# Kernel tuning notes

Hardware: AMD Instinct MI355X
Metric: run time of the kernel (lower is better)

The kernel has to match this reference:

```python
import jax, jax.numpy as jnp
import numpy as np
import math

HIDDEN = 1024
INTER = 4096
HEADS = 16
HEAD_DIM = 64
INNER = HEADS * HEAD_DIM
SEQ = 4096


def setup_inputs() -> dict:
    key = jax.random.key(0)
    ks = jax.random.split(key, 16)
    s = 0.02
    d = dict(
        x=jax.random.normal(ks[0], (SEQ, HIDDEN), dtype=jnp.float32),
        # attention norm
        an_w=jnp.ones((HIDDEN,), jnp.float32),
        an_b=jnp.zeros((HIDDEN,), jnp.float32),
        # attention projections (weight stored as [out, in] like torch)
        q_w=jax.random.normal(ks[1], (INNER, HIDDEN)) * s,
        q_b=jnp.zeros((INNER,), jnp.float32),
        k_w=jax.random.normal(ks[2], (INNER, HIDDEN)) * s,
        k_b=jnp.zeros((INNER,), jnp.float32),
        v_w=jax.random.normal(ks[3], (INNER, HIDDEN)) * s,
        v_b=jnp.zeros((INNER,), jnp.float32),
        o_w=jax.random.normal(ks[4], (HIDDEN, INNER)) * s,
        o_b=jnp.zeros((HIDDEN,), jnp.float32),
        # ff norm
        fn_w=jnp.ones((HIDDEN,), jnp.float32),
        fn_b=jnp.zeros((HIDDEN,), jnp.float32),
        ff1_w=jax.random.normal(ks[5], (INTER, HIDDEN)) * s,
        ff1_b=jnp.zeros((INTER,), jnp.float32),
        ff2_w=jax.random.normal(ks[6], (HIDDEN, INTER)) * s,
        ff2_b=jnp.zeros((HIDDEN,), jnp.float32),
    )
    return d


def _norm_novar(x, w, b):
    # mean-only layer norm (no variance normalization)
    return w * (x - jnp.mean(x, axis=-1, keepdims=True)) + b


def _block(x, an_w, an_b, q_w, q_b, k_w, k_b, v_w, v_b, o_w, o_b,
           fn_w, fn_b, ff1_w, ff1_b, ff2_w, ff2_b):
    S = x.shape[0]
    scale = math.sqrt(HEAD_DIM)
    xn = _norm_novar(x, an_w, an_b)
    # [S, inner] -> [h, S, d]
    Q = (xn @ q_w.T + q_b).reshape(S, HEADS, HEAD_DIM).transpose(1, 0, 2)
    K = (xn @ k_w.T + k_b).reshape(S, HEADS, HEAD_DIM).transpose(1, 0, 2)
    V = (xn @ v_w.T + v_b).reshape(S, HEADS, HEAD_DIM).transpose(1, 0, 2)
    scores = jnp.einsum('hsd,htd->hst', Q, K) / scale  # [h, S, S]
    attn = jax.nn.softmax(scores, axis=-1)
    ctx = jnp.einsum('hst,htd->hsd', attn, V)  # [h, S, d]
    ctx = ctx.transpose(1, 0, 2).reshape(S, INNER)
    x = ctx @ o_w.T + o_b + x
    xn = _norm_novar(x, fn_w, fn_b)
    h = jax.nn.relu(xn @ ff1_w.T + ff1_b)
    return h @ ff2_w.T + ff2_b + x


def reference(x, an_w, an_b, q_w, q_b, k_w, k_b, v_w, v_b, o_w, o_b,
              fn_w, fn_b, ff1_w, ff1_b, ff2_w, ff2_b):
    return _block(x, an_w, an_b, q_w, q_b, k_w, k_b, v_w, v_b, o_w, o_b,
                  fn_w, fn_b, ff1_w, ff1_b, ff2_w, ff2_b)
```

## Files before the change

kernel.cpp:

```cpp
#include <hip/hip_runtime.h>
#include <hip/hip_bf16.h>

#define SQ 4096
#define HID 1024
#define INTER_DIM 4096
#define NH 16
#define DH 64
#define SCALE_Q 0.18033688f

typedef __attribute__((ext_vector_type(4))) float f32x4;
typedef __attribute__((ext_vector_type(16))) float f32x16;
typedef __attribute__((ext_vector_type(8))) short bf16x8;

__device__ __forceinline__ unsigned short f2bf(float f) {
  union { float f; unsigned int i; } v; v.f = f;
  unsigned int i = v.i;
  return (unsigned short)((i + 0x7FFFu + ((i >> 16) & 1u)) >> 16);
}

__device__ __forceinline__ void load_lds16(const void* g, void* l) {
  __builtin_amdgcn_global_load_lds(
      (const __attribute__((address_space(1))) void*)g,
      (__attribute__((address_space(3))) void*)l, 16, 0, 0);
}

__device__ __forceinline__ int cvtpk_bf16(float a, float b) {
  int r;
  asm("v_cvt_pk_bf16_f32 %0, %1, %2" : "=v"(r) : "v"(a), "v"(b));
  return r;
}

__global__ __launch_bounds__(256) void cvt6_kernel(
    const float* __restrict__ s0, const float* __restrict__ s1,
    const float* __restrict__ s2, const float* __restrict__ s3,
    const float* __restrict__ s4, const float* __restrict__ s5,
    unsigned short* __restrict__ dst) {
  const int b = blockIdx.x;
  const float* src;
  int lb;
  size_t base4;
  if (b < 4096) {
    const int r = b >> 10;
    lb = b & 1023;
    src = (r == 0) ? s0 : (r == 1) ? s1 : (r == 2) ? s2 : s3;
    base4 = (size_t)r << 18;
  } else if (b < 8192) {
    lb = b - 4096; src = s4; base4 = 1u << 20;
  } else {
    lb = b - 8192; src = s5; base4 = 2u << 20;
  }
  const float sc = (b < 1024) ? SCALE_Q : 1.0f;
  const int i = lb * 256 + threadIdx.x;
  const float4 v4 = ((const float4*)src)[i];
  ushort4 o4;
  o4.x = f2bf(v4.x * sc); o4.y = f2bf(v4.y * sc);
  o4.z = f2bf(v4.z * sc); o4.w = f2bf(v4.w * sc);
  ((ushort4*)dst)[base4 + i] = o4;
}

__global__ __launch_bounds__(256) void bias3_kernel(
    const float* __restrict__ qb, const float* __restrict__ kb,
    const float* __restrict__ vb, float* __restrict__ dst) {
  const int b = blockIdx.x, t = threadIdx.x;
  const float* s = (b == 0) ? qb : (b == 1) ? kb : vb;
  float4 v = ((const float4*)s)[t];
  if (b == 0) { v.x *= SCALE_Q; v.y *= SCALE_Q; v.z *= SCALE_Q; v.w *= SCALE_Q; }
  ((float4*)dst)[b * 256 + t] = v;
}

__global__ __launch_bounds__(256) void ln_kernel(
    const float* __restrict__ x, const float* __restrict__ w,
    const float* __restrict__ b, unsigned short* __restrict__ out) {
  const int row = blockIdx.x;
  const int t = threadIdx.x;
  const float4 v = ((const float4*)(x + (size_t)row * HID))[t];
  float s = v.x + v.y + v.z + v.w;
  #pragma unroll
  for (int off = 32; off > 0; off >>= 1) s += __shfl_xor(s, off);
  __shared__ float red[4];
  if ((t & 63) == 0) red[t >> 6] = s;
  __syncthreads();
  const float mean = (red[0] + red[1] + red[2] + red[3]) * (1.0f / HID);
  const float4 wv = ((const float4*)w)[t];
  const float4 bv = ((const float4*)b)[t];
  ushort4 o;
  o.x = f2bf(wv.x * (v.x - mean) + bv.x);
  o.y = f2bf(wv.y * (v.y - mean) + bv.y);
  o.z = f2bf(wv.z * (v.z - mean) + bv.z);
  o.w = f2bf(wv.w * (v.w - mean) + bv.w);
  ((ushort4*)(out + (size_t)row * HID))[t] = o;
}

template <int MODE>
__global__ __launch_bounds__(256) void gemm_bt(
    const unsigned short* __restrict__ A, const unsigned short* __restrict__ B,
    const float* __restrict__ bias, const float* __restrict__ res,
    void* __restrict__ Cout, void* __restrict__ Cout2, int M, int N, int K) {
  __shared__ __align__(16) unsigned short As[2][128 * 32];
  __shared__ __align__(16) unsigned short Bs[2][128 * 32];
  const int t = threadIdx.x;
  const int lane = t & 63;
  const int wave = t >> 6;
  const int g = lane >> 4;
  const int lr = lane & 15;
  const int waveM = wave >> 1, waveN = wave & 1;
  const int rowBase = blockIdx.x * 128;
  const int colBase = blockIdx.y * 128;

  f32x4 acc[4][4];
  #pragma unroll
  for (int m = 0; m < 4; ++m)
    #pragma unroll
    for (int n = 0; n < 4; ++n) acc[m][n] = (f32x4){0.f, 0.f, 0.f, 0.f};

  const int c0 = t, c1 = t + 256;
  const int r0s = c0 >> 2, s0 = (c0 & 3) ^ (r0s & 3);
  const int r1s = c1 >> 2, s1 = (c1 & 3) ^ (r1s & 3);
  const unsigned short* gA0 = A + (size_t)(rowBase + r0s) * K + s0 * 8;
  const unsigned short* gA1 = A + (size_t)(rowBase + r1s) * K + s1 * 8;
  const unsigned short* gB0 = B + (size_t)(colBase + r0s) * K + s0 * 8;
  const unsigned short* gB1 = B + (size_t)(colBase + r1s) * K + s1 * 8;

  load_lds16(gA0, &As[0][wave * 512]);
  load_lds16(gA1, &As[0][2048 + wave * 512]);
  load_lds16(gB0, &Bs[0][wave * 512]);
  load_lds16(gB1, &Bs[0][2048 + wave * 512]);
  __syncthreads();

  const int nk = K >> 5;
  for (int kt = 0; kt < nk; ++kt) {
    const int buf = kt & 1;
    if (kt + 1 < nk) {
      const int k0 = (kt + 1) << 5;
      load_lds16(gA0 + k0, &As[buf ^ 1][wave * 512]);
      load_lds16(gA1 + k0, &As[buf ^ 1][2048 + wave * 512]);
      load_lds16(gB0 + k0, &Bs[buf ^ 1][wave * 512]);
      load_lds16(gB1 + k0, &Bs[buf ^ 1][2048 + wave * 512]);
    }
    bf16x8 af[4], bfr[4];
    #pragma unroll
    for (int m = 0; m < 4; ++m) {
      const int r = waveM * 64 + m * 16 + lr;
      af[m] = *(const bf16x8*)&As[buf][r * 32 + ((g ^ (r & 3)) << 3)];
    }
    #pragma unroll
    for (int n = 0; n < 4; ++n) {
      const int c = waveN * 64 + n * 16 + lr;
      bfr[n] = *(const bf16x8*)&Bs[buf][c * 32 + ((g ^ (c & 3)) << 3)];
    }
    #pragma unroll
    for (int m = 0; m < 4; ++m)
      #pragma unroll
      for (int n = 0; n < 4; ++n)
        acc[m][n] = __builtin_amdgcn_mfma_f32_16x16x32_bf16(af[m], bfr[n],
                                                            acc[m][n], 0, 0, 0);
    __syncthreads();
  }

  const int crow0 = rowBase + waveM * 64;
  const int ccol0 = colBase + waveN * 64;
  #pragma unroll
  for (int n = 0; n < 4; ++n) {
    const int col = ccol0 + n * 16 + lr;
    const float bv = bias[col];
    #pragma unroll
    for (int m = 0; m < 4; ++m) {
      const int row0 = crow0 + m * 16 + g * 4;
      if (MODE == 4) {
        if (col < 2048) {
          #pragma unroll
          for (int j = 0; j < 4; ++j)
            ((unsigned short*)Cout)[(size_t)(row0 + j) * 2048 + col] =
                f2bf(acc[m][n][j] + bv);
        } else {
          ushort4 o4;
          o4.x = f2bf(acc[m][n][0] + bv);
          o4.y = f2bf(acc[m][n][1] + bv);
          o4.z = f2bf(acc[m][n][2] + bv);
          o4.w = f2bf(acc[m][n][3] + bv);
          *(ushort4*)&((unsigned short*)Cout2)[(size_t)(col - 2048) * M + row0] = o4;
        }
      } else if (MODE == 1) {
        #pragma unroll
        for (int j = 0; j < 4; ++j)
          ((unsigned short*)Cout)[(size_t)(row0 + j) * N + col] =
              f2bf(fmaxf(acc[m][n][j] + bv, 0.f));
      } else {
        #pragma unroll
        for (int j = 0; j < 4; ++j)
          ((float*)Cout)[(size_t)(row0 + j) * N + col] =
              acc[m][n][j] + bv + res[(size_t)(row0 + j) * N + col];
      }
    }
  }
}

__global__ __launch_bounds__(256, 2) void attn_kernel(
    const unsigned short* __restrict__ QK,
    const unsigned short* __restrict__ Vt,
    unsigned short* __restrict__ ctx) {
  const int s = blockIdx.y * gridDim.x + blockIdx.x;
  const int q6 = s >> 3;
  const int h = (s & 7) * 2 + (q6 >> 5);
  const int qt = q6 & 31;

  const int t = threadIdx.x;
  const int lane = t & 63;
  const int wave = t >> 6;
  const int ql = lane & 31;
  const int hi = lane >> 5;

  __shared__ __align__(16) unsigned short Ks[2][64 * 64];
  __shared__ __align__(16) unsigned short Vs[2][64 * 64];

  const int qbase = qt * 128 + wave * 32;
  const unsigned short* qptr =
      QK + (size_t)(qbase + ql) * 2048 + h * DH + hi * 8;
  bf16x8 qf[4];
  #pragma unroll
  for (int ks = 0; ks < 4; ++ks) qf[ks] = *(const bf16x8*)(qptr + ks * 16);

  const int cr = t >> 3, cs = t & 7;
  const int cr2 = cr + 32;
  const unsigned short* gK0 =
      QK + (size_t)cr * 2048 + 1024 + h * DH + ((cs ^ (cr & 7)) << 3);
  const unsigned short* gK1 =
      QK + (size_t)cr2 * 2048 + 1024 + h * DH + ((cs ^ (cr2 & 7)) << 3);
  const unsigned short* gV0 = Vt + (size_t)(h * DH + cr) * SQ + ((cs ^ (cr & 7)) << 3);
  const unsigned short* gV1 = Vt + (size_t)(h * DH + cr2) * SQ + ((cs ^ (cr2 & 7)) << 3);

  float mreg = 0.f, lreg = 0.f;
  f32x16 oacc0 = 0.f, oacc1 = 0.f;

  load_lds16(gK0, &Ks[0][wave * 512]);
  load_lds16(gK1, &Ks[0][2048 + wave * 512]);
  load_lds16(gV0, &Vs[0][wave * 512]);
  load_lds16(gV1, &Vs[0][2048 + wave * 512]);

  for (int kt = 0; kt < SQ / 64; ++kt) {
    const int buf = kt & 1;
    __syncthreads();
    if (kt + 1 < SQ / 64) {
      const size_t ko = (size_t)(kt + 1) * 64 * 2048;
      const int vo = (kt + 1) * 64;
      load_lds16(gK0 + ko, &Ks[buf ^ 1][wave * 512]);
      load_lds16(gK1 + ko, &Ks[buf ^ 1][2048 + wave * 512]);
      load_lds16(gV0 + vo, &Vs[buf ^ 1][wave * 512]);
      load_lds16(gV1 + vo, &Vs[buf ^ 1][2048 + wave * 512]);
    }
    const unsigned short* KsB = &Ks[buf][0];
    const unsigned short* VsB = &Vs[buf][0];

    f32x16 st0, st1;
    #pragma unroll
    for (int r = 0; r < 16; ++r) { st0[r] = -mreg; st1[r] = -mreg; }
    __builtin_amdgcn_s_setprio(1);
    #pragma unroll
    for (int ks = 0; ks < 4; ++ks) {
      const int sl = ((((ks << 1) | hi) ^ (ql & 7)) << 3);
      const bf16x8 k0 = *(const bf16x8*)&KsB[ql * 64 + sl];
      const bf16x8 k1 = *(const bf16x8*)&KsB[(32 + ql) * 64 + sl];
      st0 = __builtin_amdgcn_mfma_f32_32x32x16_bf16(k0, qf[ks], st0, 0, 0, 0);
      st1 = __builtin_amdgcn_mfma_f32_32x32x16_bf16(k1, qf[ks], st1, 0, 0, 0);
    }
    __builtin_amdgcn_s_setprio(0);

    bf16x8 vf0[4], vf1[4];
    #pragma unroll
    for (int ks = 0; ks < 4; ++ks) {
      const int sl = ((((ks << 1) | hi) ^ (ql & 7)) << 3);
      vf0[ks] = *(const bf16x8*)&VsB[ql * 64 + sl];
      vf1[ks] = *(const bf16x8*)&VsB[(32 + ql) * 64 + sl];
    }

    float tr[16];
    #pragma unroll
    for (int r = 0; r < 16; ++r) tr[r] = fmaxf(st0[r], st1[r]);
    #pragma unroll
    for (int s2 = 8; s2 > 0; s2 >>= 1)
      #pragma unroll
      for (int r = 0; r < s2; ++r) tr[r] = fmaxf(tr[r], tr[r + s2]);
    const float mx = fmaxf(tr[0], __shfl_xor(tr[0], 32));

    if (!__all(mx <= 8.0f)) {
      const float mpos = fmaxf(mx, 0.f);
      const float corr = exp2f(-mpos);
      mreg += mpos;
      lreg *= corr;
      #pragma unroll
      for (int r = 0; r < 16; ++r) { st0[r] -= mpos; st1[r] -= mpos; }
      #pragma unroll
      for (int r = 0; r < 16; ++r) {
        const float c = __shfl(corr, (r & 3) + 8 * (r >> 2) + 4 * hi);
        oacc0[r] *= c;
        oacc1[r] *= c;
      }
    }

    #pragma unroll
    for (int r = 0; r < 16; ++r) st0[r] = exp2f(st0[r]);
    #pragma unroll
    for (int r = 0; r < 16; ++r) st1[r] = exp2f(st1[r]);
    float ts[16];
    #pragma unroll
    for (int r = 0; r < 16; ++r) ts[r] = st0[r] + st1[r];
    #pragma unroll
    for (int s2 = 8; s2 > 0; s2 >>= 1)
      #pragma unroll
      for (int r = 0; r < s2; ++r) ts[r] += ts[r + s2];
    lreg += ts[0] + __shfl_xor(ts[0], 32);

    union { int w[4]; bf16x8 v; } pa[4];
    #pragma unroll
    for (int half = 0; half < 2; ++half) {
      #pragma unroll
      for (int kk = 0; kk < 2; ++kk) {
        const int base = kk * 8;
        float p0, p1, p2, p3, p4, p5, p6, p7;
        if (half == 0) {
          p0 = st0[base + 0]; p1 = st0[base + 1]; p2 = st0[base + 2]; p3 = st0[base + 3];
          p4 = st0[base + 4]; p5 = st0[base + 5]; p6 = st0[base + 6]; p7 = st0[base + 7];
        } else {
          p0 = st1[base + 0]; p1 = st1[base + 1]; p2 = st1[base + 2]; p3 = st1[base + 3];
          p4 = st1[base + 4]; p5 = st1[base + 5]; p6 = st1[base + 6]; p7 = st1[base + 7];
        }
        const int d0 = cvtpk_bf16(p0, p1), sw0 = cvtpk_bf16(p4, p5);
        const int d1 = cvtpk_bf16(p2, p3), sw1 = cvtpk_bf16(p6, p7);
        auto a = __builtin_amdgcn_permlane32_swap(d0, sw0, false, false);
        auto b = __builtin_amdgcn_permlane32_swap(d1, sw1, false, false);
        const int ks = half * 2 + kk;
        pa[ks].w[0] = a[0]; pa[ks].w[1] = b[0];
        pa[ks].w[2] = a[1]; pa[ks].w[3] = b[1];
      }
    }

    __builtin_amdgcn_s_setprio(1);
    #pragma unroll
    for (int ks = 0; ks < 4; ++ks) {
      oacc0 = __builtin_amdgcn_mfma_f32_32x32x16_bf16(pa[ks].v, vf0[ks], oacc0, 0, 0, 0);
      oacc1 = __builtin_amdgcn_mfma_f32_32x32x16_bf16(pa[ks].v, vf1[ks], oacc1, 0, 0, 0);
    }
    __builtin_amdgcn_s_setprio(0);
  }

  const float linv = 1.0f / lreg;
  #pragma unroll
  for (int r = 0; r < 16; ++r) {
    const int qq = (r & 3) + 8 * (r >> 2) + 4 * hi;
    const float li = __shfl(linv, qq);
    unsigned short* cp = ctx + (size_t)(qbase + qq) * HID + h * DH + ql;
    cp[0] = f2bf(oacc0[r] * li);
    cp[32] = f2bf(oacc1[r] * li);
  }
}

extern "C" void kernel_launch(void* const* d_in, const int* in_sizes, int n_in,
                              void* d_out, int out_size, void* d_ws,
                              size_t ws_size, hipStream_t stream) {
  const float* x     = (const float*)d_in[0];
  const float* an_w  = (const float*)d_in[1];
  const float* an_b  = (const float*)d_in[2];
  const float* q_w   = (const float*)d_in[3];
  const float* q_b   = (const float*)d_in[4];
  const float* k_w   = (const float*)d_in[5];
  const float* k_b   = (const float*)d_in[6];
  const float* v_w   = (const float*)d_in[7];
  const float* v_b   = (const float*)d_in[8];
  const float* o_w   = (const float*)d_in[9];
  const float* o_b   = (const float*)d_in[10];
  const float* fn_w  = (const float*)d_in[11];
  const float* fn_b  = (const float*)d_in[12];
  const float* ff1_w = (const float*)d_in[13];
  const float* ff1_b = (const float*)d_in[14];
  const float* ff2_w = (const float*)d_in[15];
  const float* ff2_b = (const float*)d_in[16];

  char* ws = (char*)d_ws;
  const size_t MB = 1ull << 20;
  unsigned short* xn    = (unsigned short*)(ws + 0);
  unsigned short* qkvwb = (unsigned short*)(ws + 8 * MB);
  unsigned short* owb   = (unsigned short*)(ws + 14 * MB);
  unsigned short* f1wb  = (unsigned short*)(ws + 16 * MB);
  unsigned short* f2wb  = (unsigned short*)(ws + 24 * MB);
  unsigned short* QKm   = (unsigned short*)(ws + 32 * MB);
  unsigned short* Vtm   = (unsigned short*)(ws + 48 * MB);
  unsigned short* ctx   = (unsigned short*)(ws + 56 * MB);
  float*          bAll  = (float*)(ws + 56 * MB);
  float*          x2    = (float*)(ws + 64 * MB);
  unsigned short* hbuf  = (unsigned short*)(ws + 32 * MB);
  unsigned short* x2n   = xn;

  cvt6_kernel<<<12288, 256, 0, stream>>>(q_w, k_w, v_w, o_w, ff1_w, ff2_w, qkvwb);
  bias3_kernel<<<3, 256, 0, stream>>>(q_b, k_b, v_b, bAll);

  ln_kernel<<<SQ, 256, 0, stream>>>(x, an_w, an_b, xn);

  gemm_bt<4><<<dim3(SQ / 128, 3072 / 128), 256, 0, stream>>>(
      xn, qkvwb, bAll, nullptr, QKm, Vtm, SQ, 3072, HID);

  attn_kernel<<<dim3(32, 16), 256, 0, stream>>>(QKm, Vtm, ctx);

  gemm_bt<2><<<dim3(SQ / 128, HID / 128), 256, 0, stream>>>(
      ctx, owb, o_b, x, x2, nullptr, SQ, HID, HID);

  ln_kernel<<<SQ, 256, 0, stream>>>(x2, fn_w, fn_b, x2n);

  gemm_bt<1><<<dim3(SQ / 128, INTER_DIM / 128), 256, 0, stream>>>(
      x2n, f1wb, ff1_b, nullptr, hbuf, nullptr, SQ, INTER_DIM, HID);

  gemm_bt<2><<<dim3(SQ / 128, HID / 128), 256, 0, stream>>>(
      hbuf, f2wb, ff2_b, x2, (float*)d_out, nullptr, SQ, HID, INTER_DIM);
}
```

Before: 446.7 us.

## Use 256x256 GEMM tiles, split-KV attention and split-K FF2 with combine kernels

Replaces the 128x128 GEMMs for QKV and FF1 with 512-thread 256x256 tiles built on 32x32x16 MFMA. Attention is split into two KV halves, each writing unnormalized bf16 partials plus max/sum, and a combine kernel merges them. FF2 uses split-K=4 with bf16 partials, combined together with the residual. Raw v_exp_f32 replaces exp2f. This adds extra kernels and memory traffic, and bf16-rounded partials cost some accuracy in exchange for more parallelism and data reuse.

```diff
diff --git a/kernel.cpp b/kernel.cpp
--- a/kernel.cpp
+++ b/kernel.cpp
@@ -12,6 +12,9 @@
 typedef __attribute__((ext_vector_type(16))) float f32x16;
 typedef __attribute__((ext_vector_type(8))) short bf16x8;
 
+__device__ __forceinline__ float bf2f(unsigned short u) {
+  union { float f; unsigned int i; } v; v.i = ((unsigned int)u) << 16; return v.f;
+}
 __device__ __forceinline__ unsigned short f2bf(float f) {
   union { float f; unsigned int i; } v; v.f = f;
   unsigned int i = v.i;
@@ -27,6 +30,12 @@
 __device__ __forceinline__ int cvtpk_bf16(float a, float b) {
   int r;
   asm("v_cvt_pk_bf16_f32 %0, %1, %2" : "=v"(r) : "v"(a), "v"(b));
+  return r;
+}
+
+__device__ __forceinline__ float fexp2(float x) {
+  float r;
+  asm("v_exp_f32 %0, %1\n\ts_nop 1" : "=v"(r) : "v"(x));
   return r;
 }
 
@@ -92,10 +101,139 @@
 }
 
 template <int MODE>
-__global__ __launch_bounds__(256) void gemm_bt(
+__global__ __launch_bounds__(512, 1) void gemm256(
+    const unsigned short* __restrict__ A, const unsigned short* __restrict__ B,
+    const float* __restrict__ bias, void* __restrict__ C0,
+    void* __restrict__ C1, int M, int N, int K) {
+  __shared__ __align__(16) unsigned short As[2][8192];
+  __shared__ __align__(16) unsigned short Bs[2][8192];
+  const int t = threadIdx.x;
+  const int lane = t & 63;
+  const int w = t >> 6;
+  const int ql = lane & 31, hi = lane >> 5;
+  const int wm = w >> 2, wn = w & 3;
+  const int bR = blockIdx.x * 256;
+  const int bC = blockIdx.y * 256;
+  const int Keff = (MODE == 6) ? (K >> 2) : K;
+  const int kBase = (MODE == 6) ? blockIdx.z * Keff : 0;
+
+  f32x16 acc[4][2];
+  #pragma unroll
+  for (int mf = 0; mf < 4; ++mf)
+    #pragma unroll
+    for (int nf = 0; nf < 2; ++nf) acc[mf][nf] = 0.f;
+
+  const int r0 = t >> 2, s0 = (t & 3) ^ (r0 & 3);
+  const int r1 = r0 + 128, s1 = (t & 3) ^ (r1 & 3);
+  const unsigned short* gA0 = A + (size_t)(bR + r0) * K + kBase + s0 * 8;
+  const unsigned short* gA1 = A + (size_t)(bR + r1) * K + kBase + s1 * 8;
+  const unsigned short* gB0 = B + (size_t)(bC + r0) * K + kBase + s0 * 8;
+  const unsigned short* gB1 = B + (size_t)(bC + r1) * K + kBase + s1 * 8;
+
+  load_lds16(gA0, &As[0][w * 512]);
+  load_lds16(gA1, &As[0][4096 + w * 512]);
+  load_lds16(gB0, &Bs[0][w * 512]);
+  load_lds16(gB1, &Bs[0][4096 + w * 512]);
+  __syncthreads();
+
+  const int nk = Keff >> 5;
+  for (int kt = 0; kt < nk; ++kt) {
+    const int buf = kt & 1;
+    if (kt + 1 < nk) {
+      const int k0 = (kt + 1) << 5;
+      load_lds16(gA0 + k0, &As[buf ^ 1][w * 512]);
+      load_lds16(gA1 + k0, &As[buf ^ 1][4096 + w * 512]);
+      load_lds16(gB0 + k0, &Bs[buf ^ 1][w * 512]);
+      load_lds16(gB1 + k0, &Bs[buf ^ 1][4096 + w * 512]);
+    }
+    bf16x8 af[2][4], bfr[2][2];
+    #pragma unroll
+    for (int ks = 0; ks < 2; ++ks) {
+      #pragma unroll
+      for (int mf = 0; mf < 4; ++mf) {
+        const int row = wm * 128 + mf * 32 + ql;
+        af[ks][mf] = *(const bf16x8*)
+            &As[buf][row * 32 + ((ks * 16 + hi * 8) ^ ((row & 3) << 3))];
+      }
+      #pragma unroll
+      for (int nf = 0; nf < 2; ++nf) {
+        const int col = wn * 64 + nf * 32 + ql;
+        bfr[ks][nf] = *(const bf16x8*)
+            &Bs[buf][col * 32 + ((ks * 16 + hi * 8) ^ ((col & 3) << 3))];
+      }
+    }
+    __builtin_amdgcn_s_setprio(1);
+    #pragma unroll
+    for (int ks = 0; ks < 2; ++ks)
+      #pragma unroll
+      for (int mf = 0; mf < 4; ++mf)
+        #pragma unroll
+        for (int nf = 0; nf < 2; ++nf)
+          acc[mf][nf] = __builtin_amdgcn_mfma_f32_32x32x16_bf16(
+              af[ks][mf], bfr[ks][nf], acc[mf][nf], 0, 0, 0);
+    __builtin_amdgcn_s_setprio(0);
+    __syncthreads();
+  }
+
+  #pragma unroll
+  for (int mf = 0; mf < 4; ++mf) {
+    #pragma unroll
+    for (int nf = 0; nf < 2; ++nf) {
+      const int col = bC + wn * 64 + nf * 32 + ql;
+      const float bv = bias[col];
+      const int rowb = bR + wm * 128 + mf * 32;
+      if (MODE == 4) {
+        if (col < 2048) {
+          #pragma unroll
+          for (int r = 0; r < 16; ++r) {
+            const int row = rowb + (r & 3) + 8 * (r >> 2) + 4 * hi;
+            ((unsigned short*)C0)[(size_t)row * 2048 + col] =
+                f2bf(acc[mf][nf][r] + bv);
+          }
+        } else {
+          #pragma unroll
+          for (int r2 = 0; r2 < 4; ++r2) {
+            const int row = rowb + 8 * r2 + 4 * hi;
+            ushort4 o4;
+            o4.x = f2bf(acc[mf][nf][4 * r2 + 0] + bv);
+            o4.y = f2bf(acc[mf][nf][4 * r2 + 1] + bv);
+            o4.z = f2bf(acc[mf][nf][4 * r2 + 2] + bv);
+            o4.w = f2bf(acc[mf][nf][4 * r2 + 3] + bv);
+            *(ushort4*)&((unsigned short*)C1)[(size_t)(col - 2048) * M + row] = o4;
+          }
+        }
+      } else if (MODE == 1) {
+        #pragma unroll
+        for (int r = 0; r < 16; ++r) {
+          const int row = rowb + (r & 3) + 8 * (r >> 2) + 4 * hi;
+          ((unsigned short*)C0)[(size_t)row * N + col] =
+              f2bf(fmaxf(acc[mf][nf][r] + bv, 0.f));
+        }
+      } else {
+        if (blockIdx.z == 3) {
+          #pragma unroll
+          for (int r = 0; r < 16; ++r) {
+            const int row = rowb + (r & 3) + 8 * (r >> 2) + 4 * hi;
+            ((float*)C0)[(size_t)row * N + col] = acc[mf][nf][r] + bv;
+          }
+        } else {
+          unsigned short* P =
+              (unsigned short*)C1 + (size_t)blockIdx.z * M * (size_t)N;
+          #pragma unroll
+          for (int r = 0; r < 16; ++r) {
+            const int row = rowb + (r & 3) + 8 * (r >> 2) + 4 * hi;
+            P[(size_t)row * N + col] = f2bf(acc[mf][nf][r]);
+          }
+        }
+      }
+    }
+  }
+}
+
+__global__ __launch_bounds__(256) void gemm128_res(
     const unsigned short* __restrict__ A, const unsigned short* __restrict__ B,
     const float* __restrict__ bias, const float* __restrict__ res,
-    void* __restrict__ Cout, void* __restrict__ Cout2, int M, int N, int K) {
+    float* __restrict__ Cout, int M, int N, int K) {
   __shared__ __align__(16) unsigned short As[2][128 * 32];
   __shared__ __align__(16) unsigned short Bs[2][128 * 32];
   const int t = threadIdx.x;
@@ -165,43 +303,26 @@
     const float bv = bias[col];
     #pragma unroll
     for (int m = 0; m < 4; ++m) {
-      const int row0 = crow0 + m * 16 + g * 4;
-      if (MODE == 4) {
-        if (col < 2048) {
-          #pragma unroll
-          for (int j = 0; j < 4; ++j)
-            ((unsigned short*)Cout)[(size_t)(row0 + j) * 2048 + col] =
-                f2bf(acc[m][n][j] + bv);
-        } else {
-          ushort4 o4;
-          o4.x = f2bf(acc[m][n][0] + bv);
-          o4.y = f2bf(acc[m][n][1] + bv);
-          o4.z = f2bf(acc[m][n][2] + bv);
-          o4.w = f2bf(acc[m][n][3] + bv);
-          *(ushort4*)&((unsigned short*)Cout2)[(size_t)(col - 2048) * M + row0] = o4;
-        }
-      } else if (MODE == 1) {
-        #pragma unroll
-        for (int j = 0; j < 4; ++j)
-          ((unsigned short*)Cout)[(size_t)(row0 + j) * N + col] =
-              f2bf(fmaxf(acc[m][n][j] + bv, 0.f));
-      } else {
-        #pragma unroll
-        for (int j = 0; j < 4; ++j)
-          ((float*)Cout)[(size_t)(row0 + j) * N + col] =
-              acc[m][n][j] + bv + res[(size_t)(row0 + j) * N + col];
+      #pragma unroll
+      for (int j = 0; j < 4; ++j) {
+        const int row = crow0 + m * 16 + g * 4 + j;
+        Cout[(size_t)row * N + col] =
+            acc[m][n][j] + bv + res[(size_t)row * N + col];
       }
     }
   }
 }
 
-__global__ __launch_bounds__(256, 2) void attn_kernel(
+__global__ __launch_bounds__(256, 4) void attn_kernel(
     const unsigned short* __restrict__ QK,
     const unsigned short* __restrict__ Vt,
-    unsigned short* __restrict__ ctx) {
+    unsigned short* __restrict__ ctxP,
+    float2* __restrict__ ml) {
   const int s = blockIdx.y * gridDim.x + blockIdx.x;
-  const int q6 = s >> 3;
-  const int h = (s & 7) * 2 + (q6 >> 5);
+  const int kvh = s & 1;
+  const int s2 = s >> 1;
+  const int q6 = s2 >> 3;
+  const int h = (s2 & 7) * 2 + (q6 >> 5);
   const int qt = q6 & 31;
 
   const int t = threadIdx.x;
@@ -222,12 +343,15 @@
 
   const int cr = t >> 3, cs = t & 7;
   const int cr2 = cr + 32;
+  const size_t kvoff = (size_t)kvh * 2048;
   const unsigned short* gK0 =
-      QK + (size_t)cr * 2048 + 1024 + h * DH + ((cs ^ (cr & 7)) << 3);
+      QK + (kvoff + cr) * 2048 + 1024 + h * DH + ((cs ^ (cr & 7)) << 3);
   const unsigned short* gK1 =
-      QK + (size_t)cr2 * 2048 + 1024 + h * DH + ((cs ^ (cr2 & 7)) << 3);
-  const unsigned short* gV0 = Vt + (size_t)(h * DH + cr) * SQ + ((cs ^ (cr & 7)) << 3);
-  const unsigned short* gV1 = Vt + (size_t)(h * DH + cr2) * SQ + ((cs ^ (cr2 & 7)) << 3);
+      QK + (kvoff + cr2) * 2048 + 1024 + h * DH + ((cs ^ (cr2 & 7)) << 3);
+  const unsigned short* gV0 =
+      Vt + (size_t)(h * DH + cr) * SQ + kvoff + ((cs ^ (cr & 7)) << 3);
+  const unsigned short* gV1 =
+      Vt + (size_t)(h * DH + cr2) * SQ + kvoff + ((cs ^ (cr2 & 7)) << 3);
 
   float mreg = 0.f, lreg = 0.f;
   f32x16 oacc0 = 0.f, oacc1 = 0.f;
@@ -237,10 +361,11 @@
   load_lds16(gV0, &Vs[0][wave * 512]);
   load_lds16(gV1, &Vs[0][2048 + wave * 512]);
 
-  for (int kt = 0; kt < SQ / 64; ++kt) {
+  const int NT = 32;
+  for (int kt = 0; kt < NT; ++kt) {
     const int buf = kt & 1;
     __syncthreads();
-    if (kt + 1 < SQ / 64) {
+    if (kt + 1 < NT) {
       const size_t ko = (size_t)(kt + 1) * 64 * 2048;
       const int vo = (kt + 1) * 64;
       load_lds16(gK0 + ko, &Ks[buf ^ 1][wave * 512]);
@@ -277,14 +402,14 @@
     #pragma unroll
     for (int r = 0; r < 16; ++r) tr[r] = fmaxf(st0[r], st1[r]);
     #pragma unroll
-    for (int s2 = 8; s2 > 0; s2 >>= 1)
-      #pragma unroll
-      for (int r = 0; r < s2; ++r) tr[r] = fmaxf(tr[r], tr[r + s2]);
+    for (int s2_ = 8; s2_ > 0; s2_ >>= 1)
+      #pragma unroll
+      for (int r = 0; r < s2_; ++r) tr[r] = fmaxf(tr[r], tr[r + s2_]);
     const float mx = fmaxf(tr[0], __shfl_xor(tr[0], 32));
 
     if (!__all(mx <= 8.0f)) {
       const float mpos = fmaxf(mx, 0.f);
-      const float corr = exp2f(-mpos);
+      const float corr = fexp2(-mpos);
       mreg += mpos;
       lreg *= corr;
       #pragma unroll
@@ -298,16 +423,16 @@
     }
 
     #pragma unroll
-    for (int r = 0; r < 16; ++r) st0[r] = exp2f(st0[r]);
-    #pragma unroll
-    for (int r = 0; r < 16; ++r) st1[r] = exp2f(st1[r]);
+    for (int r = 0; r < 16; ++r) st0[r] = fexp2(st0[r]);
+    #pragma unroll
+    for (int r = 0; r < 16; ++r) st1[r] = fexp2(st1[r]);
     float ts[16];
     #pragma unroll
     for (int r = 0; r < 16; ++r) ts[r] = st0[r] + st1[r];
     #pragma unroll
-    for (int s2 = 8; s2 > 0; s2 >>= 1)
-      #pragma unroll
-      for (int r = 0; r < s2; ++r) ts[r] += ts[r + s2];
+    for (int s2_ = 8; s2_ > 0; s2_ >>= 1)
+      #pragma unroll
+      for (int r = 0; r < s2_; ++r) ts[r] += ts[r + s2_];
     lreg += ts[0] + __shfl_xor(ts[0], 32);
 
     union { int w[4]; bf16x8 v; } pa[4];
@@ -343,15 +468,66 @@
     __builtin_amdgcn_s_setprio(0);
   }
 
-  const float linv = 1.0f / lreg;
+  unsigned short* cpb = ctxP + (size_t)kvh * (SQ * (size_t)HID);
   #pragma unroll
   for (int r = 0; r < 16; ++r) {
     const int qq = (r & 3) + 8 * (r >> 2) + 4 * hi;
-    const float li = __shfl(linv, qq);
-    unsigned short* cp = ctx + (size_t)(qbase + qq) * HID + h * DH + ql;
-    cp[0] = f2bf(oacc0[r] * li);
-    cp[32] = f2bf(oacc1[r] * li);
-  }
+    unsigned short* cp = cpb + (size_t)(qbase + qq) * HID + h * DH + ql;
+    cp[0] = f2bf(oacc0[r]);
+    cp[32] = f2bf(oacc1[r]);
+  }
+  if (hi == 0) {
+    float2 v; v.x = mreg; v.y = lreg;
+    ml[(size_t)kvh * (SQ * NH) + (size_t)(qbase + ql) * NH + h] = v;
+  }
+}
+
+__global__ __launch_bounds__(256) void combine2_kernel(
+    const unsigned short* __restrict__ ctxP, const float2* __restrict__ ml,
+    unsigned short* __restrict__ ctx) {
+  const int i = blockIdx.x * 256 + threadIdx.x;
+  const int row = i >> 7;
+  const int dc = (i & 127) * 8;
+  const int head = dc >> 6;
+  const float2 a = ml[(size_t)row * NH + head];
+  const float2 b = ml[(size_t)(SQ + row) * NH + head];
+  const float M = fmaxf(a.x, b.x);
+  const float w0 = fexp2(a.x - M), w1 = fexp2(b.x - M);
+  const float inv = 1.0f / (w0 * a.y + w1 * b.y);
+  const size_t off = (size_t)row * HID + dc;
+  const size_t P = (size_t)SQ * HID;
+  ushort4 p0a = *(const ushort4*)&ctxP[off];
+  ushort4 p0b = *(const ushort4*)&ctxP[off + 4];
+  ushort4 p1a = *(const ushort4*)&ctxP[P + off];
+  ushort4 p1b = *(const ushort4*)&ctxP[P + off + 4];
+  ushort4 oa, ob;
+  oa.x = f2bf((w0 * bf2f(p0a.x) + w1 * bf2f(p1a.x)) * inv);
+  oa.y = f2bf((w0 * bf2f(p0a.y) + w1 * bf2f(p1a.y)) * inv);
+  oa.z = f2bf((w0 * bf2f(p0a.z) + w1 * bf2f(p1a.z)) * inv);
+  oa.w = f2bf((w0 * bf2f(p0a.w) + w1 * bf2f(p1a.w)) * inv);
+  ob.x = f2bf((w0 * bf2f(p0b.x) + w1 * bf2f(p1b.x)) * inv);
+  ob.y = f2bf((w0 * bf2f(p0b.y) + w1 * bf2f(p1b.y)) * inv);
+  ob.z = f2bf((w0 * bf2f(p0b.z) + w1 * bf2f(p1b.z)) * inv);
+  ob.w = f2bf((w0 * bf2f(p0b.w) + w1 * bf2f(p1b.w)) * inv);
+  *(ushort4*)&ctx[off] = oa;
+  *(ushort4*)&ctx[off + 4] = ob;
+}
+
+__global__ __launch_bounds__(256) void combine4_kernel(
+    float* __restrict__ out, const unsigned short* __restrict__ parts,
+    const float* __restrict__ res) {
+  const int i = blockIdx.x * 256 + threadIdx.x;
+  const size_t P = (size_t)SQ * HID;
+  float4 o = ((const float4*)out)[i];
+  const float4 r = ((const float4*)res)[i];
+  const ushort4 a = ((const ushort4*)parts)[i];
+  const ushort4 b = ((const ushort4*)(parts + P))[i];
+  const ushort4 c = ((const ushort4*)(parts + 2 * P))[i];
+  o.x += r.x + bf2f(a.x) + bf2f(b.x) + bf2f(c.x);
+  o.y += r.y + bf2f(a.y) + bf2f(b.y) + bf2f(c.y);
+  o.z += r.z + bf2f(a.z) + bf2f(b.z) + bf2f(c.z);
+  o.w += r.w + bf2f(a.w) + bf2f(b.w) + bf2f(c.w);
+  ((float4*)out)[i] = o;
 }
 
 extern "C" void kernel_launch(void* const* d_in, const int* in_sizes, int n_in,
@@ -378,6 +554,7 @@
   char* ws = (char*)d_ws;
   const size_t MB = 1ull << 20;
   unsigned short* xn    = (unsigned short*)(ws + 0);
+  float2*         mlb   = (float2*)(ws + 0);
   unsigned short* qkvwb = (unsigned short*)(ws + 8 * MB);
   unsigned short* owb   = (unsigned short*)(ws + 14 * MB);
   unsigned short* f1wb  = (unsigned short*)(ws + 16 * MB);
@@ -387,27 +564,33 @@
   unsigned short* ctx   = (unsigned short*)(ws + 56 * MB);
   float*          bAll  = (float*)(ws + 56 * MB);
   float*          x2    = (float*)(ws + 64 * MB);
+  unsigned short* ctxP  = (unsigned short*)(ws + 64 * MB);
   unsigned short* hbuf  = (unsigned short*)(ws + 32 * MB);
   unsigned short* x2n   = xn;
+  unsigned short* parts = (unsigned short*)(ws + 0);
 
   cvt6_kernel<<<12288, 256, 0, stream>>>(q_w, k_w, v_w, o_w, ff1_w, ff2_w, qkvwb);
   bias3_kernel<<<3, 256, 0, stream>>>(q_b, k_b, v_b, bAll);
 
   ln_kernel<<<SQ, 256, 0, stream>>>(x, an_w, an_b, xn);
 
-  gemm_bt<4><<<dim3(SQ / 128, 3072 / 128), 256, 0, stream>>>(
-      xn, qkvwb, bAll, nullptr, QKm, Vtm, SQ, 3072, HID);
-
-  attn_kernel<<<dim3(32, 16), 256, 0, stream>>>(QKm, Vtm, ctx);
-
-  gemm_bt<2><<<dim3(SQ / 128, HID / 128), 256, 0, stream>>>(
-      ctx, owb, o_b, x, x2, nullptr, SQ, HID, HID);
+  gemm256<4><<<dim3(SQ / 256, 3072 / 256), 512, 0, stream>>>(
+      xn, qkvwb, bAll, QKm, Vtm, SQ, 3072, HID);
+
+  attn_kernel<<<dim3(32, 32), 256, 0, stream>>>(QKm, Vtm, ctxP, mlb);
+  combine2_kernel<<<(SQ * HID / 8) / 256, 256, 0, stream>>>(ctxP, mlb, ctx);
+
+  gemm128_res<<<dim3(SQ / 128, HID / 128), 256, 0, stream>>>(
+      ctx, owb, o_b, x, x2, SQ, HID, HID);
 
   ln_kernel<<<SQ, 256, 0, stream>>>(x2, fn_w, fn_b, x2n);
 
-  gemm_bt<1><<<dim3(SQ / 128, INTER_DIM / 128), 256, 0, stream>>>(
-      x2n, f1wb, ff1_b, nullptr, hbuf, nullptr, SQ, INTER_DIM, HID);
-
-  gemm_bt<2><<<dim3(SQ / 128, HID / 128), 256, 0, stream>>>(
-      hbuf, f2wb, ff2_b, x2, (float*)d_out, nullptr, SQ, HID, INTER_DIM);
-}
+  gemm256<1><<<dim3(SQ / 256, INTER_DIM / 256), 512, 0, stream>>>(
+      x2n, f1wb, ff1_b, hbuf, nullptr, SQ, INTER_DIM, HID);
+
+  gemm256<6><<<dim3(SQ / 256, HID / 256, 4), 512, 0, stream>>>(
+      hbuf, f2wb, ff2_b, (float*)d_out, parts, SQ, HID, INTER_DIM);
+
+  combine4_kernel<<<(SQ * HID / 4) / 256, 256, 0, stream>>>(
+      (float*)d_out, parts, x2);
+}
```

New measurement: 459.7 us. 2.9% more time.
